# Optimization experiments

Hardware: AMD Instinct MI355X
Metric: run time of the kernel (lower is better)

## Reference

```python
import jax, jax.numpy as jnp
import numpy as np

B, H, W, C = 4, 256, 256, 16
NT = 9


def _rot2(a):
    c, s = np.cos(a), np.sin(a)
    return np.array([[c, -s], [s, c]])


def _aff(m2):
    p = np.eye(3)
    p[:2, :2] = m2
    return p


def _t(tx, ty):
    p = np.eye(3)
    p[0, 2] = tx
    p[1, 2] = ty
    return p


def _refl(direction):
    # reflection across line through origin spanned by `direction`
    v = np.asarray(direction, dtype=np.float64)
    m2 = 2.0 * np.outer(v, v) / np.dot(v, v) - np.eye(2)
    return _aff(m2)


def _get_transforms(t0, t1, t2):
    L = np.eye(3)
    L[:2, 0] = t1
    L[:2, 1] = t2
    L[:2, 2] = t0
    rot = lambda n: _aff(_rot2(2.0 * np.pi / n))
    e = np.eye(3)
    r2 = _t(.5, .5) @ rot(2) @ _t(-.5, -.5)
    r3 = _t(.5, .5) @ rot(3) @ _t(-.5, -.5)
    r4 = _t(.5, .5) @ rot(4) @ _t(-.5, -.5)
    r6 = _t(.5, .5) @ rot(6) @ _t(-.5, -.5)
    f_p = _t(0, .5) @ np.diag([1.0, -1.0, 1.0]) @ _t(0, -.5)
    f_c = np.array([[0.0, 1, 0], [1, 0, 0], [0, 0, 1]])
    f_l = _t(.5, .5) @ _refl(_rot2(5 * np.pi / 6) @ np.array([1.0, 0.0])) @ _t(-.5, -.5)
    f_s = _t(.5, .5) @ _refl(_rot2(np.pi / 3) @ np.array([1.0, 0.0])) @ _t(-.5, -.5)
    Ts = np.stack([e, r2, r3, r4, r6, f_p, f_c, f_l, f_s])
    Ts = L[None] @ Ts @ np.linalg.inv(L)[None]
    Ts = np.linalg.inv(Ts)
    Ts = Ts / Ts[:, 2:3, 2:3]  # normalize so last entry is 1
    return Ts.reshape(NT, 9)[:, :8].astype(np.float32)  # TF flat transform params


def setup_inputs() -> dict:
    key = jax.random.key(0)
    inputs = jax.random.normal(key, (B, H, W, C), dtype=jnp.float32)
    transforms = jnp.asarray(_get_transforms((0.0, 0.0), (float(H), 0.0), (0.0, float(W))))
    return {"inputs": inputs, "transforms": transforms}


def _warp_nearest(img, flat):
    # TF image_projective_transform_v2 semantics with NEAREST interpolation,
    # constant (zero) fill. flat maps OUTPUT (x,y) -> INPUT (x,y).
    b, h, w, c = img.shape
    yy, xx = jnp.meshgrid(jnp.arange(h, dtype=jnp.float32),
                          jnp.arange(w, dtype=jnp.float32), indexing="ij")
    a0, a1, a2, a3, a4, a5, a6, a7 = [flat[i] for i in range(8)]
    k = a6 * xx + a7 * yy + 1.0
    xi = jnp.round((a0 * xx + a1 * yy + a2) / k).astype(jnp.int32)
    yi = jnp.round((a3 * xx + a4 * yy + a5) / k).astype(jnp.int32)
    valid = (xi >= 0) & (xi < w) & (yi >= 0) & (yi < h)
    xi = jnp.clip(xi, 0, w - 1)
    yi = jnp.clip(yi, 0, h - 1)
    out = img[:, yi, xi, :]  # [b,h,w,c] gather
    return jnp.where(valid[None, :, :, None], out, 0.0)


def _forward(inputs, transforms):
    b, h, w, c = inputs.shape
    nt = transforms.shape[0]
    # warp the input by each of the nt group transforms: [nt,b,h,w,c]
    yw = jax.vmap(lambda m: _warp_nearest(inputs, m))(transforms)
    x = jnp.broadcast_to(inputs[None], yw.shape)
    x = jnp.transpose(x, (0, 1, 4, 2, 3))   # [nt,b,c,h,w]
    yw = jnp.transpose(yw, (0, 1, 4, 2, 3))
    # circular normalized cross-correlation via FFT, per channel image
    fx = jnp.fft.rfft2(x)
    fy = jnp.fft.rfft2(yw)
    corr = jnp.fft.irfft2(fx * jnp.conj(fy), s=(h, w))  # [nt,b,c,h,w]
    nx = jnp.linalg.norm(x.reshape(nt, b, c, -1), axis=-1)[..., None, None]
    ny = jnp.linalg.norm(yw.reshape(nt, b, c, -1), axis=-1)[..., None, None]
    corr = corr / (nx * ny + 1e-12)
    out = corr.mean(axis=2)                  # mean over channels -> [nt,b,h,w]
    return jnp.transpose(out, (1, 2, 3, 0))  # channels_last [b,h,w,nt]


def reference(inputs, transforms):
    return _forward(inputs, transforms)
```

## Files before the change

### kernel.cpp

```cpp
#include <hip/hip_runtime.h>
#include <hip/hip_fp16.h>

#define Bn  4
#define Hn  256
#define Wn  256
#define Cn  16
#define NTn 9
#define HWn (Hn*Wn)
#define KF  129
#define KGP 136
#define SRL 266
#define PI_F 3.14159265358979323846f

__device__ __forceinline__ int swz(int i) { return i ^ ((i >> 4) & 15); }

__device__ __forceinline__ void lds_fence() {
  __asm__ volatile("s_waitcnt lgkmcnt(0)" ::: "memory");
}

__device__ __forceinline__ float2 cmul(float2 a, float2 b) {
  return make_float2(a.x*b.x - a.y*b.y, a.x*b.y + a.y*b.x);
}

template<bool INV>
__device__ __forceinline__ void radix4(float2& x0, float2& x1, float2& x2, float2& x3) {
  float2 y0 = make_float2(x0.x + x2.x, x0.y + x2.y);
  float2 y1 = make_float2(x0.x - x2.x, x0.y - x2.y);
  float2 y2 = make_float2(x1.x + x3.x, x1.y + x3.y);
  float2 y3 = make_float2(x1.x - x3.x, x1.y - x3.y);
  x0 = make_float2(y0.x + y2.x, y0.y + y2.y);
  x2 = make_float2(y0.x - y2.x, y0.y - y2.y);
  if (!INV) {
    x1 = make_float2(y1.x + y3.y, y1.y - y3.x);
    x3 = make_float2(y1.x - y3.y, y1.y + y3.x);
  } else {
    x1 = make_float2(y1.x - y3.y, y1.y + y3.x);
    x3 = make_float2(y1.x + y3.y, y1.y - y3.x);
  }
}

struct Tw { float2 a1,a2,a3,b1,b2,b3,c1,c2,c3; };

template<bool INV>
__device__ __forceinline__ Tw make_tw(int lane) {
  const float sgn = INV ? 2.0f * PI_F : -2.0f * PI_F;
  Tw t; float sw, cw;
  __sincosf(sgn * (float)lane / 256.0f, &sw, &cw);
  t.a1 = make_float2(cw, sw); t.a2 = cmul(t.a1, t.a1); t.a3 = cmul(t.a2, t.a1);
  __sincosf(sgn * (float)(lane & 15) / 64.0f, &sw, &cw);
  t.b1 = make_float2(cw, sw); t.b2 = cmul(t.b1, t.b1); t.b3 = cmul(t.b2, t.b1);
  __sincosf(sgn * (float)(lane & 3) / 16.0f, &sw, &cw);
  t.c1 = make_float2(cw, sw); t.c2 = cmul(t.c1, t.c1); t.c3 = cmul(t.c2, t.c1);
  return t;
}

template<bool INV, int NF>
__device__ __forceinline__ void fft256_n(float2 (*v)[4], float2 (*s)[SRL],
                                         int lane, const Tw& t) {
#pragma unroll
  for (int f = 0; f < NF; ++f) {
    radix4<INV>(v[f][0], v[f][1], v[f][2], v[f][3]);
    v[f][1] = cmul(v[f][1], t.a1); v[f][2] = cmul(v[f][2], t.a2); v[f][3] = cmul(v[f][3], t.a3);
#pragma unroll
    for (int a = 0; a < 4; ++a) s[f][swz(lane + (a << 6))] = v[f][a];
  }
  lds_fence();
  { int base = (lane >> 4) * 64 + (lane & 15);
#pragma unroll
    for (int f = 0; f < NF; ++f)
#pragma unroll
      for (int a = 0; a < 4; ++a) v[f][a] = s[f][swz(base + (a << 4))];
  }
  lds_fence();
#pragma unroll
  for (int f = 0; f < NF; ++f) {
    radix4<INV>(v[f][0], v[f][1], v[f][2], v[f][3]);
    v[f][1] = cmul(v[f][1], t.b1); v[f][2] = cmul(v[f][2], t.b2); v[f][3] = cmul(v[f][3], t.b3);
    int base = (lane >> 4) * 64 + (lane & 15);
#pragma unroll
    for (int a = 0; a < 4; ++a) s[f][swz(base + (a << 4))] = v[f][a];
  }
  lds_fence();
  { int base = (lane >> 4) * 64 + ((lane >> 2) & 3) * 16 + (lane & 3);
#pragma unroll
    for (int f = 0; f < NF; ++f)
#pragma unroll
      for (int a = 0; a < 4; ++a) v[f][a] = s[f][swz(base + (a << 2))];
  }
  lds_fence();
#pragma unroll
  for (int f = 0; f < NF; ++f) {
    radix4<INV>(v[f][0], v[f][1], v[f][2], v[f][3]);
    v[f][1] = cmul(v[f][1], t.c1); v[f][2] = cmul(v[f][2], t.c2); v[f][3] = cmul(v[f][3], t.c3);
    int base = (lane & ~3) * 4 + (lane & 3);
#pragma unroll
    for (int a = 0; a < 4; ++a) s[f][swz(base + (a << 2))] = v[f][a];
  }
  lds_fence();
  { int base = lane * 4;
#pragma unroll
    for (int f = 0; f < NF; ++f)
#pragma unroll
      for (int a = 0; a < 4; ++a) v[f][a] = s[f][swz(base + a)];
  }
  lds_fence();
  int dr = ((lane & 3) << 4) + (((lane >> 2) & 3) << 2) + (lane >> 4);
#pragma unroll
  for (int f = 0; f < NF; ++f) {
    radix4<INV>(v[f][0], v[f][1], v[f][2], v[f][3]);
#pragma unroll
    for (int a = 0; a < 4; ++a) s[f][swz(dr + (a << 6))] = v[f][a];
  }
  lds_fence();
}

__device__ __forceinline__ int warp_id(float a0, float a1, float a2, float a3,
                                       float a4, float a5, float a6, float a7,
                                       int col, int row) {
#pragma clang fp contract(off)
  float x = (float)col, y = (float)row;
  float kk = a6 * x + a7 * y + 1.0f;
  float xf = (a0 * x + a1 * y + a2) / kk;
  float yf = (a3 * x + a4 * y + a5) / kk;
  float xr = rintf(xf), yr = rintf(yf);
  bool valid = (xr >= 0.f) && (xr < 256.f) && (yr >= 0.f) && (yr < 256.f);
  return valid ? ((int)yr * Wn + (int)xr) : -1;
}

__global__ __launch_bounds__(256) void k_yrow(const float* __restrict__ inp,
                                              const float* __restrict__ T,
                                              __half2* __restrict__ Yh,
                                              float* __restrict__ part) {
  __shared__ float2 sb[4][4][SRL];
  __shared__ float4 redw[4];
  int tid = threadIdx.x, w = tid >> 6, lane = tid & 63;
  Tw t = make_tw<false>(lane);
  int chunk = blockIdx.x & 15, cg = (blockIdx.x >> 4) & 3, tb = blockIdx.x >> 6;
  int b = tb & 3, tt = tb >> 2;
  int i0 = chunk << 4;
  const float4* ib = (const float4*)(inp + (size_t)b * HWn * Cn);
  float a0, a1, a2, a3, a4, a5, a6, a7;
  { const float* a = T + tt * 8;
    a0=a[0]; a1=a[1]; a2=a[2]; a3=a[3]; a4=a[4]; a5=a[5]; a6=a[6]; a7=a[7]; }
  float4 nyacc = make_float4(0.f, 0.f, 0.f, 0.f);
  for (int h = 0; h < 2; ++h) {
    if (h) __syncthreads();
    int r0 = i0 + h * 8 + 2 * w;
    float4 g0[4], g1[4];
#pragma unroll
    for (int q = 0; q < 4; ++q) {
      int col = lane + (q << 6);
      int id0 = warp_id(a0,a1,a2,a3,a4,a5,a6,a7, col, r0);
      int id1 = warp_id(a0,a1,a2,a3,a4,a5,a6,a7, col, r0 + 1);
      g0[q] = (id0 >= 0) ? ib[(size_t)id0 * 4 + cg] : make_float4(0.f,0.f,0.f,0.f);
      g1[q] = (id1 >= 0) ? ib[(size_t)id1 * 4 + cg] : make_float4(0.f,0.f,0.f,0.f);
      nyacc.x += g0[q].x*g0[q].x + g1[q].x*g1[q].x;
      nyacc.y += g0[q].y*g0[q].y + g1[q].y*g1[q].y;
      nyacc.z += g0[q].z*g0[q].z + g1[q].z*g1[q].z;
      nyacc.w += g0[q].w*g0[q].w + g1[q].w*g1[q].w;
    }
    float2 v[4][4];
#pragma unroll
    for (int q = 0; q < 4; ++q) {
      v[0][q] = make_float2(g0[q].x, g1[q].x);
      v[1][q] = make_float2(g0[q].y, g1[q].y);
      v[2][q] = make_float2(g0[q].z, g1[q].z);
      v[3][q] = make_float2(g0[q].w, g1[q].w);
    }
    fft256_n<false, 4>(v, sb[w], lane, t);
    __syncthreads();
    int ii = tid & 7, kq = tid >> 3;
    int w2 = ii >> 1, odd = ii & 1;
#pragma unroll
    for (int p = 0; p < 5; ++p) {
      int k = p * 32 + kq;
      if (k <= 128) {
        int kc = (256 - k) & 255;
#pragma unroll
        for (int cc = 0; cc < 4; ++cc) {
          float2 Z  = sb[w2][cc][swz(k)];
          float2 Zc = sb[w2][cc][swz(kc)];
          float2 F = odd ? make_float2(0.5f * (Z.y + Zc.y), 0.5f * (Zc.x - Z.x))
                         : make_float2(0.5f * (Z.x + Zc.x), 0.5f * (Z.y - Zc.y));
          Yh[((size_t)(tb * Cn + cg * 4 + cc) * KF + k) * Hn + i0 + h * 8 + ii] =
              __float22half2_rn(F);
        }
      }
    }
  }
#pragma unroll
  for (int o = 32; o > 0; o >>= 1) {
    nyacc.x += __shfl_down(nyacc.x, o, 64);
    nyacc.y += __shfl_down(nyacc.y, o, 64);
    nyacc.z += __shfl_down(nyacc.z, o, 64);
    nyacc.w += __shfl_down(nyacc.w, o, 64);
  }
  if (lane == 0) redw[w] = nyacc;
  __syncthreads();
  if (tid == 0) {
    float4 s = make_float4(redw[0].x + redw[1].x + redw[2].x + redw[3].x,
                           redw[0].y + redw[1].y + redw[2].y + redw[3].y,
                           redw[0].z + redw[1].z + redw[2].z + redw[3].z,
                           redw[0].w + redw[1].w + redw[2].w + redw[3].w);
    part[((size_t)tb * Cn + cg * 4 + 0) * 16 + chunk] = s.x;
    part[((size_t)tb * Cn + cg * 4 + 1) * 16 + chunk] = s.y;
    part[((size_t)tb * Cn + cg * 4 + 2) * 16 + chunk] = s.z;
    part[((size_t)tb * Cn + cg * 4 + 3) * 16 + chunk] = s.w;
  }
}

__global__ __launch_bounds__(256) void k_colfft_fx(const __half2* __restrict__ Yh,
                                                   __half2* __restrict__ Fxh) {
  __shared__ float2 sb[4][4][SRL];
  int tid = threadIdx.x, w = tid >> 6, lane = tid & 63;
  Tw t = make_tw<false>(lane);
  int base_item = blockIdx.x * 16 + w * 4;
  float2 v[4][4];
#pragma unroll
  for (int f = 0; f < 4; ++f) {
    const __half2* Sp = Yh + (size_t)(base_item + f) * Hn;
#pragma unroll
    for (int q = 0; q < 4; ++q) v[f][q] = __half22float2(Sp[lane + (q << 6)]);
  }
  fft256_n<false, 4>(v, sb[w], lane, t);
#pragma unroll
  for (int f = 0; f < 4; ++f) {
    __half2* Op = Fxh + (size_t)(base_item + f) * Hn;
#pragma unroll
    for (int q = 0; q < 4; ++q) {
      int j = lane + (q << 6);
      Op[j] = __float22half2_rn(sb[w][f][swz(j)]);
    }
  }
}

__global__ __launch_bounds__(256) void k_ycol(const __half2* __restrict__ Yh,
                                              const __half2* __restrict__ Fxh,
                                              const float* __restrict__ part,
                                              float2* __restrict__ G) {
  __shared__ float2 sb[4][2][SRL];
  __shared__ float scs[16];
  int tid = threadIdx.x, w = tid >> 6, lane = tid & 63;
  int tb = blockIdx.x / 33, quart = blockIdx.x % 33;
  int b = tb & 3;
  if (tid < 16) {
    float sx = 0.f, sy = 0.f;
#pragma unroll
    for (int ch = 0; ch < 16; ++ch) {
      sx += part[((size_t)b  * Cn + tid) * 16 + ch];
      sy += part[((size_t)tb * Cn + tid) * 16 + ch];
    }
    scs[tid] = 1.0f / ((float)Cn * (sqrtf(sx) * sqrtf(sy) + 1e-12f));
  }
  __syncthreads();
  int k = quart * 4 + w;
  bool act = (k <= 128);
  if (act) {
    Tw tf = make_tw<false>(lane);
    float2 acc[4];
#pragma unroll
    for (int q = 0; q < 4; ++q) acc[q] = make_float2(0.f, 0.f);
    for (int c = 0; c < Cn; c += 2) {
      float2 v2[2][4];
#pragma unroll
      for (int e = 0; e < 2; ++e) {
        const __half2* Yp = Yh + ((size_t)(tb * Cn + c + e) * KF + k) * Hn;
#pragma unroll
        for (int q = 0; q < 4; ++q) v2[e][q] = __half22float2(Yp[lane + (q << 6)]);
      }
      fft256_n<false, 2>(v2, sb[w], lane, tf);
#pragma unroll
      for (int e = 0; e < 2; ++e) {
        float sc = scs[c + e];
        const __half2* Fxp = Fxh + ((size_t)(b * Cn + c + e) * KF + k) * Hn;
#pragma unroll
        for (int q = 0; q < 4; ++q) {
          int rr = lane + (q << 6);
          float2 fy = sb[w][e][swz(rr)];
          float2 fx = __half22float2(Fxp[rr]);
          acc[q].x += sc * (fx.x * fy.x + fx.y * fy.y);
          acc[q].y += sc * (fx.y * fy.x - fx.x * fy.y);
        }
      }
    }
    Tw ti = make_tw<true>(lane);
    fft256_n<true, 1>(reinterpret_cast<float2(*)[4]>(acc), sb[w], lane, ti);
  }
  __syncthreads();
  int kk = tid & 3, jj0 = tid >> 2;
  if (quart * 4 + kk <= 128) {
    float2* Gp = G + ((size_t)tb * Hn) * KGP + quart * 4 + kk;
#pragma unroll
    for (int p = 0; p < 4; ++p) {
      int j = jj0 + (p << 6);
      Gp[(size_t)j * KGP] = sb[kk][0][swz(j)];
    }
  }
}

__global__ __launch_bounds__(320) void k_irow(const float2* __restrict__ G,
                                              float* __restrict__ out) {
  __shared__ float2 tile[5][2][132];
  __shared__ float2 sb[5][SRL];
  __shared__ float rowbuf[Wn * NTn];
  int tid = threadIdx.x, w = tid >> 6, lane = tid & 63;
  Tw ti = make_tw<true>(lane);
  int b = blockIdx.x >> 8, i = blockIdx.x & 255;
  const float scale = 1.0f / ((float)Hn * (float)Wn);
  int t1 = 2 * w, t2 = t1 + 1;
  {
    const float2* Gp1 = G + ((size_t)(t1 * Bn + b) * Hn + i) * KGP;
    for (int k = lane; k < KF; k += 64) tile[w][0][k] = Gp1[k];
    if (t2 < NTn) {
      const float2* Gp2 = G + ((size_t)(t2 * Bn + b) * Hn + i) * KGP;
      for (int k = lane; k < KF; k += 64) tile[w][1][k] = Gp2[k];
    }
  }
  lds_fence();
  float2 v[1][4];
#pragma unroll
  for (int q = 0; q < 4; ++q) {
    int k = lane + (q << 6);
    float2 a, bb;
    if (k <= 128) a = tile[w][0][k];
    else { float2 z = tile[w][0][256 - k]; a = make_float2(z.x, -z.y); }
    if (t2 < NTn) {
      if (k <= 128) bb = tile[w][1][k];
      else { float2 z = tile[w][1][256 - k]; bb = make_float2(z.x, -z.y); }
    } else bb = make_float2(0.f, 0.f);
    v[0][q] = make_float2(a.x - bb.y, a.y + bb.x);
  }
  fft256_n<true, 1>(v, reinterpret_cast<float2(*)[SRL]>(sb[w]), lane, ti);
#pragma unroll
  for (int q = 0; q < 4; ++q) {
    int j = lane + (q << 6);
    float2 r = sb[w][swz(j)];
    rowbuf[j * NTn + t1] = r.x * scale;
    if (t2 < NTn) rowbuf[j * NTn + t2] = r.y * scale;
  }
  __syncthreads();
  float* ob = out + ((size_t)(b * Hn + i) * Wn) * NTn;
  for (int f = tid; f < Wn * NTn; f += 320) ob[f] = rowbuf[f];
}

extern "C" void kernel_launch(void* const* d_in, const int* in_sizes, int n_in,
                              void* d_out, int out_size, void* d_ws, size_t ws_size,
                              hipStream_t stream) {
  const float* inp = (const float*)d_in[0];
  const float* T   = (const float*)d_in[1];
  float* out = (float*)d_out;
  char* ws = (char*)d_ws;

  size_t off = 0;
  float*   part = (float*)(ws + off);  off += (size_t)NTn * Bn * Cn * 16 * sizeof(float);
  __half2* Fxh = (__half2*)(ws + off); off += (size_t)Bn * Cn * KF * Hn * sizeof(__half2);
  float2*  G   = (float2*)(ws + off);  off += (size_t)NTn * Bn * Hn * KGP * sizeof(float2);
  __half2* Yh  = (__half2*)(ws + off); off += (size_t)NTn * Bn * Cn * KF * Hn * sizeof(__half2);
  (void)off; (void)ws_size; (void)in_sizes; (void)n_in; (void)out_size;

  k_yrow<<<NTn * Bn * 64, 256, 0, stream>>>(inp, T, Yh, part);
  k_colfft_fx<<<Bn * Cn * KF / 4 / 4, 256, 0, stream>>>(Yh, Fxh);
  k_ycol<<<NTn * Bn * 33, 256, 0, stream>>>(Yh, Fxh, part, G);
  k_irow<<<Bn * Hn, 320, 0, stream>>>(G, out);
}
```

Baseline: 193.0 us.

## Split warp gather into separate kernel writing fp16 warped images

Moves the nearest-neighbour warp gather out of the row-FFT kernel into a new kernel. That kernel reads all 16 channels per pixel in full 64-byte rows and writes a channels-last fp16 warped image. The row-FFT kernel then reads this buffer instead of doing scattered 16-byte gathers once per channel group. The aim is to replace poorly coalesced gathers with contiguous reads. The cost is an extra kernel launch, a write and re-read of about 19 MB of intermediate data, and fp16 rounding of inputs before the norm and FFT.

```diff
diff --git a/kernel.cpp b/kernel.cpp
--- a/kernel.cpp
+++ b/kernel.cpp
@@ -127,45 +127,65 @@
   return valid ? ((int)yr * Wn + (int)xr) : -1;
 }
 
-__global__ __launch_bounds__(256) void k_yrow(const float* __restrict__ inp,
-                                              const float* __restrict__ T,
+__global__ __launch_bounds__(256) void k_gather(const float* __restrict__ inp,
+                                                const float* __restrict__ T,
+                                                __half* __restrict__ Wh) {
+  int tb = blockIdx.x >> 8;
+  int p = ((blockIdx.x & 255) << 8) + threadIdx.x;
+  int b = tb & 3, tt = tb >> 2;
+  int i = p >> 8, j = p & 255;
+  const float* a = T + tt * 8;
+  int id = warp_id(a[0],a[1],a[2],a[3],a[4],a[5],a[6],a[7], j, i);
+  const float4* ib = (const float4*)(inp + (size_t)b * HWn * Cn);
+  float4 x0, x1, x2, x3;
+  if (id >= 0) {
+    const float4* pp = ib + (size_t)id * 4;
+    x0 = pp[0]; x1 = pp[1]; x2 = pp[2]; x3 = pp[3];
+  } else {
+    x0 = x1 = x2 = x3 = make_float4(0.f, 0.f, 0.f, 0.f);
+  }
+  union { __half2 h[8]; float4 f[2]; } u;
+  u.h[0] = __floats2half2_rn(x0.x, x0.y); u.h[1] = __floats2half2_rn(x0.z, x0.w);
+  u.h[2] = __floats2half2_rn(x1.x, x1.y); u.h[3] = __floats2half2_rn(x1.z, x1.w);
+  u.h[4] = __floats2half2_rn(x2.x, x2.y); u.h[5] = __floats2half2_rn(x2.z, x2.w);
+  u.h[6] = __floats2half2_rn(x3.x, x3.y); u.h[7] = __floats2half2_rn(x3.z, x3.w);
+  float4* dst = (float4*)(Wh + ((size_t)tb * HWn + p) * Cn);
+  dst[0] = u.f[0];
+  dst[1] = u.f[1];
+}
+
+__global__ __launch_bounds__(256) void k_yfft(const __half* __restrict__ Wh,
                                               __half2* __restrict__ Yh,
                                               float* __restrict__ part) {
   __shared__ float2 sb[4][4][SRL];
   __shared__ float4 redw[4];
   int tid = threadIdx.x, w = tid >> 6, lane = tid & 63;
   Tw t = make_tw<false>(lane);
-  int chunk = blockIdx.x & 15, cg = (blockIdx.x >> 4) & 3, tb = blockIdx.x >> 6;
-  int b = tb & 3, tt = tb >> 2;
+  int chunk = blockIdx.x & 15, cq = (blockIdx.x >> 4) & 3, tb = blockIdx.x >> 6;
   int i0 = chunk << 4;
-  const float4* ib = (const float4*)(inp + (size_t)b * HWn * Cn);
-  float a0, a1, a2, a3, a4, a5, a6, a7;
-  { const float* a = T + tt * 8;
-    a0=a[0]; a1=a[1]; a2=a[2]; a3=a[3]; a4=a[4]; a5=a[5]; a6=a[6]; a7=a[7]; }
+  const __half2* wp = (const __half2*)(Wh + (size_t)tb * HWn * Cn);
   float4 nyacc = make_float4(0.f, 0.f, 0.f, 0.f);
   for (int h = 0; h < 2; ++h) {
     if (h) __syncthreads();
     int r0 = i0 + h * 8 + 2 * w;
-    float4 g0[4], g1[4];
+    float2 v[4][4];
 #pragma unroll
     for (int q = 0; q < 4; ++q) {
-      int col = lane + (q << 6);
-      int id0 = warp_id(a0,a1,a2,a3,a4,a5,a6,a7, col, r0);
-      int id1 = warp_id(a0,a1,a2,a3,a4,a5,a6,a7, col, r0 + 1);
-      g0[q] = (id0 >= 0) ? ib[(size_t)id0 * 4 + cg] : make_float4(0.f,0.f,0.f,0.f);
-      g1[q] = (id1 >= 0) ? ib[(size_t)id1 * 4 + cg] : make_float4(0.f,0.f,0.f,0.f);
-      nyacc.x += g0[q].x*g0[q].x + g1[q].x*g1[q].x;
-      nyacc.y += g0[q].y*g0[q].y + g1[q].y*g1[q].y;
-      nyacc.z += g0[q].z*g0[q].z + g1[q].z*g1[q].z;
-      nyacc.w += g0[q].w*g0[q].w + g1[q].w*g1[q].w;
-    }
-    float2 v[4][4];
-#pragma unroll
-    for (int q = 0; q < 4; ++q) {
-      v[0][q] = make_float2(g0[q].x, g1[q].x);
-      v[1][q] = make_float2(g0[q].y, g1[q].y);
-      v[2][q] = make_float2(g0[q].z, g1[q].z);
-      v[3][q] = make_float2(g0[q].w, g1[q].w);
+      int j = lane + (q << 6);
+      __half2 p00 = wp[(size_t)(((r0    ) << 8) + j) * 8 + cq * 2    ];
+      __half2 p01 = wp[(size_t)(((r0    ) << 8) + j) * 8 + cq * 2 + 1];
+      __half2 p10 = wp[(size_t)(((r0 + 1) << 8) + j) * 8 + cq * 2    ];
+      __half2 p11 = wp[(size_t)(((r0 + 1) << 8) + j) * 8 + cq * 2 + 1];
+      float2 f00 = __half22float2(p00), f01 = __half22float2(p01);
+      float2 f10 = __half22float2(p10), f11 = __half22float2(p11);
+      v[0][q] = make_float2(f00.x, f10.x);
+      v[1][q] = make_float2(f00.y, f10.y);
+      v[2][q] = make_float2(f01.x, f11.x);
+      v[3][q] = make_float2(f01.y, f11.y);
+      nyacc.x += f00.x*f00.x + f10.x*f10.x;
+      nyacc.y += f00.y*f00.y + f10.y*f10.y;
+      nyacc.z += f01.x*f01.x + f11.x*f11.x;
+      nyacc.w += f01.y*f01.y + f11.y*f11.y;
     }
     fft256_n<false, 4>(v, sb[w], lane, t);
     __syncthreads();
@@ -182,7 +202,7 @@
           float2 Zc = sb[w2][cc][swz(kc)];
           float2 F = odd ? make_float2(0.5f * (Z.y + Zc.y), 0.5f * (Zc.x - Z.x))
                          : make_float2(0.5f * (Z.x + Zc.x), 0.5f * (Z.y - Zc.y));
-          Yh[((size_t)(tb * Cn + cg * 4 + cc) * KF + k) * Hn + i0 + h * 8 + ii] =
+          Yh[((size_t)(tb * Cn + cq * 4 + cc) * KF + k) * Hn + i0 + h * 8 + ii] =
               __float22half2_rn(F);
         }
       }
@@ -202,10 +222,10 @@
                            redw[0].y + redw[1].y + redw[2].y + redw[3].y,
                            redw[0].z + redw[1].z + redw[2].z + redw[3].z,
                            redw[0].w + redw[1].w + redw[2].w + redw[3].w);
-    part[((size_t)tb * Cn + cg * 4 + 0) * 16 + chunk] = s.x;
-    part[((size_t)tb * Cn + cg * 4 + 1) * 16 + chunk] = s.y;
-    part[((size_t)tb * Cn + cg * 4 + 2) * 16 + chunk] = s.z;
-    part[((size_t)tb * Cn + cg * 4 + 3) * 16 + chunk] = s.w;
+    part[((size_t)tb * Cn + cq * 4 + 0) * 16 + chunk] = s.x;
+    part[((size_t)tb * Cn + cq * 4 + 1) * 16 + chunk] = s.y;
+    part[((size_t)tb * Cn + cq * 4 + 2) * 16 + chunk] = s.z;
+    part[((size_t)tb * Cn + cq * 4 + 3) * 16 + chunk] = s.w;
   }
 }
 
@@ -355,11 +375,13 @@
   float*   part = (float*)(ws + off);  off += (size_t)NTn * Bn * Cn * 16 * sizeof(float);
   __half2* Fxh = (__half2*)(ws + off); off += (size_t)Bn * Cn * KF * Hn * sizeof(__half2);
   float2*  G   = (float2*)(ws + off);  off += (size_t)NTn * Bn * Hn * KGP * sizeof(float2);
+  __half*  Wh  = (__half*)(ws + off);  off += (size_t)NTn * Bn * HWn * Cn * sizeof(__half);
   __half2* Yh  = (__half2*)(ws + off); off += (size_t)NTn * Bn * Cn * KF * Hn * sizeof(__half2);
   (void)off; (void)ws_size; (void)in_sizes; (void)n_in; (void)out_size;
 
-  k_yrow<<<NTn * Bn * 64, 256, 0, stream>>>(inp, T, Yh, part);
-  k_colfft_fx<<<Bn * Cn * KF / 4 / 4, 256, 0, stream>>>(Yh, Fxh);
+  k_gather<<<NTn * Bn * 256, 256, 0, stream>>>(inp, T, Wh);
+  k_yfft<<<NTn * Bn * 64, 256, 0, stream>>>(Wh, Yh, part);
+  k_colfft_fx<<<Bn * Cn * KF / 16, 256, 0, stream>>>(Yh, Fxh);
   k_ycol<<<NTn * Bn * 33, 256, 0, stream>>>(Yh, Fxh, part, G);
   k_irow<<<Bn * Hn, 320, 0, stream>>>(G, out);
 }
```

Result: slower. 206.3 us (+6.9%).
